# Optimization experiments

Measured on AMD Instinct MI355X. Metric: run time of the kernel, lower is better.

The kernel has to match this reference:

```python
import jax, jax.numpy as jnp
import numpy as np
from jax import lax

N_STEPS = 64  # fixed-step RK4 stands in for torchdiffeq's adaptive dopri5
INPUT_DIM = 64
HIDDEN_DIM = 256
BATCH = 262144


def setup_inputs() -> dict:
    key = jax.random.key(0)
    k_x, k_t, k_w1, k_b1, k_w2, k_b2 = jax.random.split(key, 6)
    x = jax.random.normal(k_x, (BATCH, INPUT_DIM), dtype=jnp.float32)
    t = jax.random.uniform(k_t, (1,), dtype=jnp.float32, minval=0.1, maxval=1.0)
    # torch Linear convention: y = x @ W.T + b
    s1 = 1.0 / np.sqrt(INPUT_DIM)
    s2 = 1.0 / np.sqrt(HIDDEN_DIM)
    W1 = jax.random.uniform(k_w1, (HIDDEN_DIM, INPUT_DIM), jnp.float32, -s1, s1)
    b1 = jax.random.uniform(k_b1, (HIDDEN_DIM,), jnp.float32, -s1, s1)
    W2 = jax.random.uniform(k_w2, (INPUT_DIM, HIDDEN_DIM), jnp.float32, -s2, s2)
    b2 = jax.random.uniform(k_b2, (INPUT_DIM,), jnp.float32, -s2, s2)
    return {"x": x, "t": t, "W1": W1, "b1": b1, "W2": W2, "b2": b2}


def reference(x, t, W1, b1, W2, b2):
    # ODE dynamics: f(y) = Linear2(ELU(Linear1(y))) -- autonomous (no t dependence)
    def f(y):
        h = jax.nn.elu(y @ W1.T + b1)  # [B, H]
        return h @ W2.T + b2           # [B, D]

    t0 = jnp.reshape(t, (-1,))[0]      # t.squeeze(); integrate over [0, t0]
    dt = t0 / N_STEPS

    def step(y, _):
        k1 = f(y)
        k2 = f(y + 0.5 * dt * k1)
        k3 = f(y + 0.5 * dt * k2)
        k4 = f(y + dt * k3)
        y_next = y + (dt / 6.0) * (k1 + 2.0 * k2 + 2.0 * k3 + k4)
        return y_next, None

    y_final, _ = lax.scan(step, x, None, length=N_STEPS)
    return y_final  # out[-1]: state at time t0
```

## Files before the change

### kernel.cpp

```cpp
#include <hip/hip_runtime.h>

#define NSTEP 64

typedef short bf8 __attribute__((ext_vector_type(8)));
typedef float f32x16 __attribute__((ext_vector_type(16)));
typedef float f32x4 __attribute__((ext_vector_type(4)));
typedef float f32x2 __attribute__((ext_vector_type(2)));
typedef unsigned int u32x4 __attribute__((ext_vector_type(4)));
typedef unsigned int u32x2 __attribute__((ext_vector_type(2)));

static __device__ __forceinline__ float asf(unsigned int u){ return __builtin_bit_cast(float, u); }
static __device__ __forceinline__ unsigned int asu(float f){ return __builtin_bit_cast(unsigned int, f); }

#if defined(__has_builtin)
#if __has_builtin(__builtin_amdgcn_cvt_pk_bf16_f32)
#define HAVE_CVT_PK_BF16 1
#endif
#endif
#ifdef HAVE_CVT_PK_BF16
typedef __bf16 bf16x2_t __attribute__((ext_vector_type(2)));
static __device__ __forceinline__ unsigned int pk(float a, float b){
  bf16x2_t r = __builtin_amdgcn_cvt_pk_bf16_f32(a, b);
  return __builtin_bit_cast(unsigned int, r);
}
#else
static __device__ __forceinline__ unsigned int pk(float a, float b){
  unsigned int ua = asu(a); unsigned int ub = asu(b);
  ua += 0x7FFFu + ((ua >> 16) & 1u);
  ub += 0x7FFFu + ((ub >> 16) & 1u);
  return (ua >> 16) | (ub & 0xFFFF0000u);
}
#endif

static __device__ __forceinline__ float bfr(float w){ return asf(pk(w, 0.0f) << 16); }

static __device__ __forceinline__ f32x2 pkfma(f32x2 a, f32x2 b, f32x2 c){
  return __builtin_elementwise_fma(a, b, c);
}

static __device__ __forceinline__ f32x2 pairof(const f32x16& v, int j){
  f32x2 r; r.x = v[2*j]; r.y = v[2*j+1]; return r;
}
static __device__ __forceinline__ void setpair(f32x16& v, int j, f32x2 p){
  v[2*j] = p.x; v[2*j+1] = p.y;
}

static __device__ __forceinline__ bf8 scale_bf8(bf8 w, float s){
  u32x4 u = __builtin_bit_cast(u32x4, w);
  u32x4 r;
  #pragma unroll
  for(int i=0;i<4;i++){
    float lo = asf(u[i] << 16) * s;
    float hi = asf(u[i] & 0xFFFF0000u) * s;
    r[i] = pk(lo, hi);
  }
  return __builtin_bit_cast(bf8, r);
}

#define MFMA16 __builtin_amdgcn_mfma_f32_16x16x32_bf16


#define ELU2(A, H0, H1) { \
  f32x2 q0; q0.x=A[0]; q0.y=A[1]; \
  f32x2 q1; q1.x=A[2]; q1.y=A[3]; \
  f32x2 m0 = __builtin_elementwise_max(q0, Z2); \
  f32x2 n0 = __builtin_elementwise_min(q0, Z2); \
  f32x2 m1 = __builtin_elementwise_max(q1, Z2); \
  f32x2 n1 = __builtin_elementwise_min(q1, Z2); \
  f32x2 e0; e0.x=__builtin_amdgcn_exp2f(n0.x); e0.y=__builtin_amdgcn_exp2f(n0.y); \
  f32x2 e1; e1.x=__builtin_amdgcn_exp2f(n1.x); e1.y=__builtin_amdgcn_exp2f(n1.y); \
  f32x2 h0 = pkfma(m0, LN22, e0); \
  f32x2 h1 = pkfma(m1, LN22, e1); \
  H0 = pk(h0.x, h0.y); H1 = pk(h1.x, h1.y); \
}

#define CHUNK0 { \
  f32x4 a0 = MFMA16(W1f[0][0], zf0, b1r[0], 0,0,0); \
  a0       = MFMA16(W1f[0][1], zf1, a0,     0,0,0); \
  f32x4 a1 = MFMA16(W1f[1][0], zf0, b1r[1], 0,0,0); \
  a1       = MFMA16(W1f[1][1], zf1, a1,     0,0,0); \
  unsigned int H00,H01,H10,H11; \
  ELU2(a0, H00, H01) \
  ELU2(a1, H10, H11) \
  u32x4 hu; hu[0]=H00; hu[1]=H01; hu[2]=H10; hu[3]=H11; \
  bf8 hf = __builtin_bit_cast(bf8, hu); \
  p2[0] = MFMA16(W2f[0][0], hf, b2r[0], 0,0,0); \
  p2[1] = MFMA16(W2f[1][0], hf, b2r[1], 0,0,0); \
  p2[2] = MFMA16(W2f[2][0], hf, b2r[2], 0,0,0); \
  p2[3] = MFMA16(W2f[3][0], hf, b2r[3], 0,0,0); \
}
#define CHUNKN(KT) { \
  f32x4 a0 = MFMA16(W1f[2*(KT)  ][0], zf0, b1r[2*(KT)],   0,0,0); \
  a0       = MFMA16(W1f[2*(KT)  ][1], zf1, a0,            0,0,0); \
  f32x4 a1 = MFMA16(W1f[2*(KT)+1][0], zf0, b1r[2*(KT)+1], 0,0,0); \
  a1       = MFMA16(W1f[2*(KT)+1][1], zf1, a1,            0,0,0); \
  unsigned int H00,H01,H10,H11; \
  ELU2(a0, H00, H01) \
  ELU2(a1, H10, H11) \
  u32x4 hu; hu[0]=H00; hu[1]=H01; hu[2]=H10; hu[3]=H11; \
  bf8 hf = __builtin_bit_cast(bf8, hu); \
  p2[0] = MFMA16(W2f[0][KT], hf, p2[0], 0,0,0); \
  p2[1] = MFMA16(W2f[1][KT], hf, p2[1], 0,0,0); \
  p2[2] = MFMA16(W2f[2][KT], hf, p2[2], 0,0,0); \
  p2[3] = MFMA16(W2f[3][KT], hf, p2[3], 0,0,0); \
}

__global__ __launch_bounds__(128, 2) void ode_kernel(
    const void* __restrict__ xv,
    const void* __restrict__ tv,
    const void* __restrict__ W1v,
    const void* __restrict__ b1v,
    const void* __restrict__ W2v,
    const void* __restrict__ b2v,
    void* __restrict__ outv)
{
  __shared__ __align__(16) float b1s[256];
  __shared__ __align__(16) float b2s[64];
  __shared__ __align__(16) float xbuf[2][2][1024];

  const int tid = threadIdx.x;
  const int lid = tid & 63;
  const int wv  = tid >> 6;

  const unsigned int* w1u = (const unsigned int*)W1v;
  bool bad = false;
  #pragma unroll
  for(int i=0; i<2; i++){
    unsigned int d = w1u[i*64 + lid];
    unsigned int e0 = (d >> 7)  & 0xFFu;
    unsigned int e1 = (d >> 23) & 0xFFu;
    bad |= (e0 >= 125u) || (e1 >= 125u);
  }
  const bool f32in = (__ballot(bad) != 0ull);

  const float L2E = 1.4426950408889634f;

  if(f32in){
    #pragma unroll
    for(int i=0; i<2; i++) b1s[tid + i*128] = ((const float*)b1v)[tid + i*128] * L2E;
  } else {
    #pragma unroll
    for(int i=0; i<2; i++)
      b1s[tid + i*128] = asf((unsigned int)((const unsigned short*)b1v)[tid + i*128] << 16) * L2E;
  }
  if(tid < 64){
    float ssum = 0.0f;
    if(f32in){
      const float* W2 = (const float*)W2v + tid*256;
      #pragma unroll 4
      for(int k=0; k<64; k++){
        f32x4 w4 = *(const f32x4*)(W2 + k*4);
        ssum += bfr(w4[0]) + bfr(w4[1]) + bfr(w4[2]) + bfr(w4[3]);
      }
    } else {
      const unsigned short* W2 = (const unsigned short*)W2v + tid*256;
      for(int k=0; k<256; k++) ssum += asf((unsigned int)W2[k] << 16);
    }
    float bb = f32in ? ((const float*)b2v)[tid]
                     : asf((unsigned int)((const unsigned short*)b2v)[tid] << 16);
    b2s[tid] = (bb - ssum) * 0.5f;
  }
  __syncthreads();

  const int ln = lid & 15;
  const int g  = lid >> 4;
  const int g4 = g * 4;
  const int rr = blockIdx.x * 16 + ln;

  const float t  = f32in ? ((const float*)tv)[0]
                         : asf((unsigned int)((const unsigned short*)tv)[0] << 16);
  const float dt  = t / (float)NSTEP;
  const float hdt = 0.5f * dt;
  const float gg  = dt * (1.0f/6.0f);
  const f32x2 DT2  = {dt, dt};
  const f32x2 HDT2 = {hdt, hdt};
  const f32x2 TWO2 = {2.0f, 2.0f};
  const f32x2 G2   = {gg, gg};
  const f32x2 LN22 = {0.6931471805599453f, 0.6931471805599453f};
  const f32x2 Z2   = {0.0f, 0.0f};

  f32x4 b1r[8];
  #pragma unroll
  for(int tl=0; tl<8; tl++) b1r[tl] = *(const f32x4*)&b1s[wv*128 + tl*16 + g4];
  f32x4 b2r[4];
  #pragma unroll
  for(int mt=0; mt<4; mt++) b2r[mt] = *(const f32x4*)&b2s[mt*16 + g4];

  bf8 W1f[8][2];
  bf8 W2f[4][4];
  if(f32in){
    const float* W1 = (const float*)W1v;
    const float* W2 = (const float*)W2v;
    #pragma unroll
    for(int mtl=0; mtl<8; mtl++){
      #pragma unroll
      for(int ks=0; ks<2; ks++){
        const float* p = W1 + (wv*128 + mtl*16 + ln)*64 + ks*32 + g4;
        f32x4 a = *(const f32x4*)p;
        f32x4 b = *(const f32x4*)(p + 16);
        u32x4 u;
        u[0]=pk(a[0]*L2E, a[1]*L2E); u[1]=pk(a[2]*L2E, a[3]*L2E);
        u[2]=pk(b[0]*L2E, b[1]*L2E); u[3]=pk(b[2]*L2E, b[3]*L2E);
        W1f[mtl][ks] = __builtin_bit_cast(bf8, u);
      }
    }
    #pragma unroll
    for(int mt=0; mt<4; mt++){
      #pragma unroll
      for(int kt=0; kt<4; kt++){
        const float* p = W2 + (mt*16 + ln)*256 + wv*128 + kt*32 + g4;
        f32x4 a = *(const f32x4*)p;
        f32x4 b = *(const f32x4*)(p + 16);
        u32x4 u; u[0]=pk(a[0],a[1]); u[1]=pk(a[2],a[3]); u[2]=pk(b[0],b[1]); u[3]=pk(b[2],b[3]);
        W2f[mt][kt] = __builtin_bit_cast(bf8, u);
      }
    }
  } else {
    const unsigned short* W1 = (const unsigned short*)W1v;
    const unsigned short* W2 = (const unsigned short*)W2v;
    #pragma unroll
    for(int mtl=0; mtl<8; mtl++){
      #pragma unroll
      for(int ks=0; ks<2; ks++){
        const unsigned short* p = W1 + (wv*128 + mtl*16 + ln)*64 + ks*32 + g4;
        u32x2 lo = *(const u32x2*)p;
        u32x2 hi = *(const u32x2*)(p + 16);
        u32x4 u; u[0]=lo[0]; u[1]=lo[1]; u[2]=hi[0]; u[3]=hi[1];
        W1f[mtl][ks] = scale_bf8(__builtin_bit_cast(bf8, u), L2E);
      }
    }
    #pragma unroll
    for(int mt=0; mt<4; mt++){
      #pragma unroll
      for(int kt=0; kt<4; kt++){
        const unsigned short* p = W2 + (mt*16 + ln)*256 + wv*128 + kt*32 + g4;
        u32x2 lo = *(const u32x2*)p;
        u32x2 hi = *(const u32x2*)(p + 16);
        u32x4 u; u[0]=lo[0]; u[1]=lo[1]; u[2]=hi[0]; u[3]=hi[1];
        W2f[mt][kt] = __builtin_bit_cast(bf8, u);
      }
    }
  }

  f32x16 Y;
  if(f32in){
    const float* x = (const float*)xv;
    #pragma unroll
    for(int mt=0; mt<4; mt++){
      f32x4 v = *(const f32x4*)(x + rr*64 + mt*16 + g4);
      #pragma unroll
      for(int i=0;i<4;i++) Y[4*mt+i] = v[i];
    }
  } else {
    const unsigned short* x = (const unsigned short*)xv;
    #pragma unroll
    for(int mt=0; mt<4; mt++){
      u32x2 v = *(const u32x2*)(x + rr*64 + mt*16 + g4);
      Y[4*mt+0]=asf(v[0]<<16); Y[4*mt+1]=asf(v[0]&0xFFFF0000u);
      Y[4*mt+2]=asf(v[1]<<16); Y[4*mt+3]=asf(v[1]&0xFFFF0000u);
    }
  }

  bf8 zf0, zf1;
  {
    u32x4 u0, u1;
    #pragma unroll
    for(int j=0;j<4;j++){
      f32x2 a = pairof(Y, j);     u0[j] = pk(a.x, a.y);
      f32x2 b = pairof(Y, j+4);   u1[j] = pk(b.x, b.y);
    }
    zf0 = __builtin_bit_cast(bf8, u0);
    zf1 = __builtin_bit_cast(bf8, u1);
  }

  int par = 0;

  #pragma unroll 1
  for(int step=0; step<NSTEP; step++){
    f32x16 A;

    #pragma unroll
    for(int s=0; s<4; s++){
      f32x4 p2[4];
      CHUNK0 CHUNKN(1) CHUNKN(2) CHUNKN(3)

      {
        float* my = &xbuf[par][wv][0];
        #pragma unroll
        for(int mt=0; mt<4; mt++)
          *(f32x4*)&my[(mt*64 + lid)*4] = p2[mt];
        __syncthreads();
        const float* prr = &xbuf[par][1-wv][0];
        u32x4 u0, u1;
        #pragma unroll
        for(int mt=0; mt<4; mt++){
          f32x4 v = *(const f32x4*)&prr[(mt*64 + lid)*4];
          f32x2 s0; s0.x = p2[mt][0]+v[0]; s0.y = p2[mt][1]+v[1];
          f32x2 s1; s1.x = p2[mt][2]+v[2]; s1.y = p2[mt][3]+v[3];
          if(s == 0){
            setpair(A, 2*mt, s0); setpair(A, 2*mt+1, s1);
          } else if(s == 3){
            setpair(A, 2*mt,   pairof(A, 2*mt)   + s0);
            setpair(A, 2*mt+1, pairof(A, 2*mt+1) + s1);
          } else {
            setpair(A, 2*mt,   pkfma(TWO2, s0, pairof(A, 2*mt)));
            setpair(A, 2*mt+1, pkfma(TWO2, s1, pairof(A, 2*mt+1)));
          }
          if(s < 3){
            const f32x2 cn = (s==2) ? DT2 : HDT2;
            f32x2 z0 = pkfma(cn, s0, pairof(Y, 2*mt));
            f32x2 z1 = pkfma(cn, s1, pairof(Y, 2*mt+1));
            if(mt < 2){ u0[2*mt] = pk(z0.x, z0.y); u0[2*mt+1] = pk(z1.x, z1.y); }
            else      { u1[2*(mt-2)] = pk(z0.x, z0.y); u1[2*(mt-2)+1] = pk(z1.x, z1.y); }
          }
        }
        if(s < 3){
          zf0 = __builtin_bit_cast(bf8, u0);
          zf1 = __builtin_bit_cast(bf8, u1);
        }
        par ^= 1;
      }
    }

    u32x4 u0, u1;
    #pragma unroll
    for(int j=0;j<8;j++){
      f32x2 y = pkfma(G2, pairof(A, j), pairof(Y, j));
      setpair(Y, j, y);
      if(j < 4) u0[j] = pk(y.x, y.y);
      else      u1[j-4] = pk(y.x, y.y);
    }
    zf0 = __builtin_bit_cast(bf8, u0);
    zf1 = __builtin_bit_cast(bf8, u1);
  }

  if(wv == 0){
    if(f32in){
      float* out = (float*)outv;
      #pragma unroll
      for(int mt=0; mt<4; mt++){
        f32x4 v;
        #pragma unroll
        for(int i=0;i<4;i++) v[i] = Y[4*mt+i];
        *(f32x4*)(out + rr*64 + mt*16 + g4) = v;
      }
    } else {
      unsigned short* out = (unsigned short*)outv;
      #pragma unroll
      for(int mt=0; mt<4; mt++){
        u32x2 v;
        v[0] = pk(Y[4*mt+0], Y[4*mt+1]);
        v[1] = pk(Y[4*mt+2], Y[4*mt+3]);
        *(u32x2*)(out + rr*64 + mt*16 + g4) = v;
      }
    }
  }
}

extern "C" void kernel_launch(void* const* d_in, const int* in_sizes, int n_in,
                              void* d_out, int out_size, void* d_ws, size_t ws_size,
                              hipStream_t stream){
  hipLaunchKernelGGL(ode_kernel, dim3(16384), dim3(128), 0, stream,
                     d_in[0], d_in[1], d_in[2], d_in[3], d_in[4], d_in[5], d_out);
}
```

Before: 6.981 ms.

## Reorder MFMA stages, raise wave priority, fold RK4 update into last stage

Splits each RK4 stage into all four GEMM1+ELU chunks first, then the GEMM2 MFMA chains per output tile. The per-tile LDS stores are interleaved with those chains. The compute section is wrapped in s_setprio(1)/s_setprio(0) so the two co-resident waves stagger their MFMA and sync phases. The final y update for the step is folded into the s==3 reduction, which removes a separate pass over the accumulators. Keeping all four hidden fragments live raises register pressure, which could matter under launch_bounds(128,2).

```diff
diff --git a/kernel.cpp b/kernel.cpp
--- a/kernel.cpp
+++ b/kernel.cpp
@@ -74,36 +74,18 @@
   H0 = pk(h0.x, h0.y); H1 = pk(h1.x, h1.y); \
 }
 
-#define CHUNK0 { \
-  f32x4 a0 = MFMA16(W1f[0][0], zf0, b1r[0], 0,0,0); \
-  a0       = MFMA16(W1f[0][1], zf1, a0,     0,0,0); \
-  f32x4 a1 = MFMA16(W1f[1][0], zf0, b1r[1], 0,0,0); \
-  a1       = MFMA16(W1f[1][1], zf1, a1,     0,0,0); \
-  unsigned int H00,H01,H10,H11; \
-  ELU2(a0, H00, H01) \
-  ELU2(a1, H10, H11) \
-  u32x4 hu; hu[0]=H00; hu[1]=H01; hu[2]=H10; hu[3]=H11; \
-  bf8 hf = __builtin_bit_cast(bf8, hu); \
-  p2[0] = MFMA16(W2f[0][0], hf, b2r[0], 0,0,0); \
-  p2[1] = MFMA16(W2f[1][0], hf, b2r[1], 0,0,0); \
-  p2[2] = MFMA16(W2f[2][0], hf, b2r[2], 0,0,0); \
-  p2[3] = MFMA16(W2f[3][0], hf, b2r[3], 0,0,0); \
-}
-#define CHUNKN(KT) { \
-  f32x4 a0 = MFMA16(W1f[2*(KT)  ][0], zf0, b1r[2*(KT)],   0,0,0); \
-  a0       = MFMA16(W1f[2*(KT)  ][1], zf1, a0,            0,0,0); \
-  f32x4 a1 = MFMA16(W1f[2*(KT)+1][0], zf0, b1r[2*(KT)+1], 0,0,0); \
-  a1       = MFMA16(W1f[2*(KT)+1][1], zf1, a1,            0,0,0); \
-  unsigned int H00,H01,H10,H11; \
-  ELU2(a0, H00, H01) \
-  ELU2(a1, H10, H11) \
-  u32x4 hu; hu[0]=H00; hu[1]=H01; hu[2]=H10; hu[3]=H11; \
-  bf8 hf = __builtin_bit_cast(bf8, hu); \
-  p2[0] = MFMA16(W2f[0][KT], hf, p2[0], 0,0,0); \
-  p2[1] = MFMA16(W2f[1][KT], hf, p2[1], 0,0,0); \
-  p2[2] = MFMA16(W2f[2][KT], hf, p2[2], 0,0,0); \
-  p2[3] = MFMA16(W2f[3][KT], hf, p2[3], 0,0,0); \
-}
+#define GEMM1ELU(KT, HF) \
+  bf8 HF; { \
+    f32x4 a0 = MFMA16(W1f[2*(KT)  ][0], zf0, b1r[2*(KT)],   0,0,0); \
+    a0       = MFMA16(W1f[2*(KT)  ][1], zf1, a0,            0,0,0); \
+    f32x4 a1 = MFMA16(W1f[2*(KT)+1][0], zf0, b1r[2*(KT)+1], 0,0,0); \
+    a1       = MFMA16(W1f[2*(KT)+1][1], zf1, a1,            0,0,0); \
+    unsigned int H00,H01,H10,H11; \
+    ELU2(a0, H00, H01) \
+    ELU2(a1, H10, H11) \
+    u32x4 hu; hu[0]=H00; hu[1]=H01; hu[2]=H10; hu[3]=H11; \
+    HF = __builtin_bit_cast(bf8, hu); \
+  }
 
 __global__ __launch_bounds__(128, 2) void ode_kernel(
     const void* __restrict__ xv,
@@ -281,15 +263,24 @@
 
     #pragma unroll
     for(int s=0; s<4; s++){
+      __builtin_amdgcn_s_setprio(1);
+      GEMM1ELU(0, hf0) GEMM1ELU(1, hf1) GEMM1ELU(2, hf2) GEMM1ELU(3, hf3)
+
+      float* my = &xbuf[par][wv][0];
       f32x4 p2[4];
-      CHUNK0 CHUNKN(1) CHUNKN(2) CHUNKN(3)
+      #pragma unroll
+      for(int mt=0; mt<4; mt++){
+        f32x4 p = MFMA16(W2f[mt][0], hf0, b2r[mt], 0,0,0);
+        p       = MFMA16(W2f[mt][1], hf1, p,       0,0,0);
+        p       = MFMA16(W2f[mt][2], hf2, p,       0,0,0);
+        p       = MFMA16(W2f[mt][3], hf3, p,       0,0,0);
+        p2[mt] = p;
+        *(f32x4*)&my[(mt*64 + lid)*4] = p;
+      }
+      __builtin_amdgcn_s_setprio(0);
+      __syncthreads();
 
       {
-        float* my = &xbuf[par][wv][0];
-        #pragma unroll
-        for(int mt=0; mt<4; mt++)
-          *(f32x4*)&my[(mt*64 + lid)*4] = p2[mt];
-        __syncthreads();
         const float* prr = &xbuf[par][1-wv][0];
         u32x4 u0, u1;
         #pragma unroll
@@ -297,41 +288,37 @@
           f32x4 v = *(const f32x4*)&prr[(mt*64 + lid)*4];
           f32x2 s0; s0.x = p2[mt][0]+v[0]; s0.y = p2[mt][1]+v[1];
           f32x2 s1; s1.x = p2[mt][2]+v[2]; s1.y = p2[mt][3]+v[3];
+          f32x2 z0, z1;
           if(s == 0){
             setpair(A, 2*mt, s0); setpair(A, 2*mt+1, s1);
-          } else if(s == 3){
-            setpair(A, 2*mt,   pairof(A, 2*mt)   + s0);
-            setpair(A, 2*mt+1, pairof(A, 2*mt+1) + s1);
-          } else {
+            z0 = pkfma(HDT2, s0, pairof(Y, 2*mt));
+            z1 = pkfma(HDT2, s1, pairof(Y, 2*mt+1));
+          } else if(s == 1){
             setpair(A, 2*mt,   pkfma(TWO2, s0, pairof(A, 2*mt)));
             setpair(A, 2*mt+1, pkfma(TWO2, s1, pairof(A, 2*mt+1)));
+            z0 = pkfma(HDT2, s0, pairof(Y, 2*mt));
+            z1 = pkfma(HDT2, s1, pairof(Y, 2*mt+1));
+          } else if(s == 2){
+            setpair(A, 2*mt,   pkfma(TWO2, s0, pairof(A, 2*mt)));
+            setpair(A, 2*mt+1, pkfma(TWO2, s1, pairof(A, 2*mt+1)));
+            z0 = pkfma(DT2, s0, pairof(Y, 2*mt));
+            z1 = pkfma(DT2, s1, pairof(Y, 2*mt+1));
+          } else {
+            f32x2 a0f = pairof(A, 2*mt)   + s0;
+            f32x2 a1f = pairof(A, 2*mt+1) + s1;
+            z0 = pkfma(G2, a0f, pairof(Y, 2*mt));
+            z1 = pkfma(G2, a1f, pairof(Y, 2*mt+1));
+            setpair(Y, 2*mt,   z0);
+            setpair(Y, 2*mt+1, z1);
           }
-          if(s < 3){
-            const f32x2 cn = (s==2) ? DT2 : HDT2;
-            f32x2 z0 = pkfma(cn, s0, pairof(Y, 2*mt));
-            f32x2 z1 = pkfma(cn, s1, pairof(Y, 2*mt+1));
-            if(mt < 2){ u0[2*mt] = pk(z0.x, z0.y); u0[2*mt+1] = pk(z1.x, z1.y); }
-            else      { u1[2*(mt-2)] = pk(z0.x, z0.y); u1[2*(mt-2)+1] = pk(z1.x, z1.y); }
-          }
+          if(mt < 2){ u0[2*mt] = pk(z0.x, z0.y); u0[2*mt+1] = pk(z1.x, z1.y); }
+          else      { u1[2*(mt-2)] = pk(z0.x, z0.y); u1[2*(mt-2)+1] = pk(z1.x, z1.y); }
         }
-        if(s < 3){
-          zf0 = __builtin_bit_cast(bf8, u0);
-          zf1 = __builtin_bit_cast(bf8, u1);
-        }
+        zf0 = __builtin_bit_cast(bf8, u0);
+        zf1 = __builtin_bit_cast(bf8, u1);
         par ^= 1;
       }
     }
-
-    u32x4 u0, u1;
-    #pragma unroll
-    for(int j=0;j<8;j++){
-      f32x2 y = pkfma(G2, pairof(A, j), pairof(Y, j));
-      setpair(Y, j, y);
-      if(j < 4) u0[j] = pk(y.x, y.y);
-      else      u1[j-4] = pk(y.x, y.y);
-    }
-    zf0 = __builtin_bit_cast(bf8, u0);
-    zf1 = __builtin_bit_cast(bf8, u1);
   }
 
   if(wv == 0){
```

After: 6.673 ms. -4.4%, faster.
